# Kernel optimization log

Measured on AMD Instinct MI355X. Metric: run time of the kernel, lower is better.

## Reference

```python
import jax, jax.numpy as jnp
import numpy as np

BN_EPS = 1e-5


def _pool_features(labels, fx, fy, n_labels):
    # Mean-pool per-pixel features (fx, fy, xx, yy coord maps) over superpixel labels.
    B, _, w, h = labels.shape
    xx = (jnp.arange(w, dtype=jnp.float32) / (w - 1)) * 2.0 - 1.0   # varies along dim 2
    yy = (jnp.arange(h, dtype=jnp.float32) / (h - 1)) * 2.0 - 1.0   # varies along dim 3
    xx_map = jnp.broadcast_to(xx[:, None], (w, h))
    yy_map = jnp.broadcast_to(yy[None, :], (w, h))
    P = w * h
    feats = jnp.stack([
        fx[:, 0].reshape(B, P),
        fy[:, 0].reshape(B, P),
        jnp.broadcast_to(xx_map.reshape(1, P), (B, P)),
        jnp.broadcast_to(yy_map.reshape(1, P), (B, P)),
    ], axis=-1).reshape(B * P, 4)                                   # [B*P, 4]
    seg = (labels[:, 0].reshape(B, P)
           + n_labels * jnp.arange(B, dtype=jnp.int32)[:, None]).reshape(-1)
    sums = jax.ops.segment_sum(feats, seg, num_segments=B * n_labels)        # [B*K, 4]
    counts = jax.ops.segment_sum(jnp.ones((B * P,), jnp.float32), seg,
                                 num_segments=B * n_labels)                  # [B*K]
    return sums / jnp.maximum(counts, 1.0)[:, None]


def _bn(x, g, b):
    # BatchNorm1d in training mode: batch statistics over the token dim.
    m = x.mean(axis=0)
    v = x.var(axis=0)
    return (x - m) * jax.lax.rsqrt(v + BN_EPS) * g + b


def reference(labels, fx, fy, frame_idx, n_frames, n_labels,
              conv_w, conv_b, bn1_g, bn1_b, lin_w, lin_b, bn2_g, bn2_b):
    pooled = _pool_features(labels, fx, fy, n_labels)               # [B*K, 4] = (fx, fy, xx, yy)
    t = jnp.repeat(frame_idx.astype(jnp.float32) / (n_frames - 1), n_labels)  # [B*K]
    x = jnp.concatenate([t[:, None], pooled], axis=1)               # [B*K, 5]
    x = x @ conv_w.T + conv_b                                       # Conv1d(5,64,1) == linear
    x = jax.nn.relu(_bn(x, bn1_g, bn1_b))
    x = x @ lin_w.T + lin_b                                         # Linear(64,32)
    x = jax.nn.relu(_bn(x, bn2_g, bn2_b))
    nrm = jnp.linalg.norm(x, axis=1, keepdims=True)
    return x / jnp.maximum(nrm, 1e-8)


def setup_inputs() -> dict:
    key = jax.random.key(0)
    ks = jax.random.split(key, 12)
    B, H, W, K = 16, 512, 512, 1024
    labels = jax.random.randint(ks[0], (B, 1, H, W), 0, K, dtype=jnp.int32)
    fx = jax.random.normal(ks[1], (B, 1, H, W), dtype=jnp.float32)
    fy = jax.random.normal(ks[2], (B, 1, H, W), dtype=jnp.float32)
    frame_idx = jax.random.randint(ks[3], (B,), 0, 100, dtype=jnp.int32)
    conv_w = jax.random.normal(ks[4], (64, 5), dtype=jnp.float32) * 0.3
    conv_b = jax.random.normal(ks[5], (64,), dtype=jnp.float32) * 0.05
    bn1_g = 1.0 + 0.05 * jax.random.normal(ks[6], (64,), dtype=jnp.float32)
    bn1_b = 0.05 * jax.random.normal(ks[7], (64,), dtype=jnp.float32)
    lin_w = jax.random.normal(ks[8], (32, 64), dtype=jnp.float32) * 0.1
    lin_b = jax.random.normal(ks[9], (32,), dtype=jnp.float32) * 0.05
    bn2_g = 1.0 + 0.05 * jax.random.normal(ks[10], (32,), dtype=jnp.float32)
    bn2_b = 0.05 * jax.random.normal(ks[11], (32,), dtype=jnp.float32)
    return {"labels": labels, "fx": fx, "fy": fy, "frame_idx": frame_idx,
            "n_frames": 100, "n_labels": K,
            "conv_w": conv_w, "conv_b": conv_b, "bn1_g": bn1_g, "bn1_b": bn1_b,
            "lin_w": lin_w, "lin_b": lin_b, "bn2_g": bn2_g, "bn2_b": bn2_b}
```

## Files before the change

kernel.cpp:

```cpp
#include <hip/hip_runtime.h>
#include <math.h>

#define TPB 256
#define TPBP 1024
#define FSCALE 16384.0f
#define INV_FSCALE (1.0f / 16384.0f)
#define FBIAS (1 << 17)
#define FCLAMP 7.0f


__global__ __launch_bounds__(TPBP)
void pool_kernel(const int* __restrict__ labels,
                 const float* __restrict__ fx,
                 const float* __restrict__ fy,
                 float* __restrict__ partial,
                 float* __restrict__ ctrl,
                 int K, int H, int W, int wlog, int chunks) {
    extern __shared__ unsigned long long sh[];
    unsigned long long* geo = sh;
    unsigned long long* fxy = sh + K;
    const int tid = threadIdx.x;

    if (blockIdx.x == 0 && tid < 224) ctrl[tid] = 0.f;

    for (int i = tid; i < K; i += TPBP) { geo[i] = 0ull; fxy[i] = 0ull; }
    __syncthreads();

    const int P = H * W;
    const int b = blockIdx.x / chunks;
    const int chunk = blockIdx.x - b * chunks;
    const int chunkP = P / chunks;
    const size_t base = (size_t)b * P + (size_t)chunk * chunkP;
    const int4*   l4p  = (const int4*)(labels + base);
    const float4* fx4p = (const float4*)(fx + base);
    const float4* fy4p = (const float4*)(fy + base);
    const int nvec = chunkP >> 2;

    for (int v = tid; v < nvec; v += TPBP) {
        int4   l4 = l4p[v];
        float4 f4 = fx4p[v];
        float4 g4 = fy4p[v];
        int p0 = chunk * chunkP + (v << 2);
        int   ls[4] = {l4.x, l4.y, l4.z, l4.w};
        float fs[4] = {f4.x, f4.y, f4.z, f4.w};
        float gs[4] = {g4.x, g4.y, g4.z, g4.w};
        #pragma unroll
        for (int s = 0; s < 4; ++s) {
            int p = p0 + s;
            int i, j;
            if (wlog >= 0) { i = p >> wlog; j = p & (W - 1); }
            else           { i = p / W;     j = p - i * W; }
            unsigned long long gadd = ((unsigned long long)i << 40)
                                    | ((unsigned long long)j << 16) | 1ull;
            int qx = __float2int_rn(fminf(fmaxf(fs[s], -FCLAMP), FCLAMP) * FSCALE) + FBIAS;
            int qy = __float2int_rn(fminf(fmaxf(gs[s], -FCLAMP), FCLAMP) * FSCALE) + FBIAS;
            unsigned long long fadd = ((unsigned long long)(unsigned int)qx << 32)
                                    | (unsigned long long)(unsigned int)qy;
            atomicAdd(&geo[ls[s]], gadd);
            atomicAdd(&fxy[ls[s]], fadd);
        }
    }
    __syncthreads();

    const float sx = 2.f / (float)(H - 1);
    const float sy = 2.f / (float)(W - 1);
    float* outp = partial + (size_t)blockIdx.x * K * 5;
    for (int k = tid; k < K; k += TPBP) {
        unsigned long long g = geo[k];
        unsigned long long ff = fxy[k];
        unsigned int ci = (unsigned int)(g & 0xFFFFull);
        float cnt = (float)ci;
        float sj  = (float)(unsigned int)((g >> 16) & 0xFFFFFFull);
        float si  = (float)(unsigned int)(g >> 40);
        long long cbias = (long long)ci << 17;
        float* p = outp + k * 5;
        p[0] = (float)((long long)(ff >> 32) - cbias) * INV_FSCALE;
        p[1] = (float)((long long)(ff & 0xFFFFFFFFull) - cbias) * INV_FSCALE;
        p[2] = sx * si - cnt;
        p[3] = sy * sj - cnt;
        p[4] = cnt;
    }
}

__device__ __forceinline__ void grid_sync(int* cnt, int nblk) {
    __syncthreads();
    if (threadIdx.x == 0) {
        __hip_atomic_fetch_add(cnt, 1, __ATOMIC_RELEASE, __HIP_MEMORY_SCOPE_AGENT);
        while (__hip_atomic_load(cnt, __ATOMIC_RELAXED, __HIP_MEMORY_SCOPE_AGENT) < nblk)
            __builtin_amdgcn_s_sleep(8);
        __hip_atomic_load(cnt, __ATOMIC_ACQUIRE, __HIP_MEMORY_SCOPE_AGENT);
    }
    __syncthreads();
}

__global__ __launch_bounds__(TPB)
void fused234_kernel(const float* __restrict__ partial,
                     const int* __restrict__ frame_idx,
                     const int* __restrict__ n_frames_p,
                     const float* __restrict__ conv_w,
                     const float* __restrict__ conv_b,
                     const float* __restrict__ bn1_g,
                     const float* __restrict__ bn1_b,
                     const float* __restrict__ lin_w,
                     const float* __restrict__ lin_b,
                     const float* __restrict__ bn2_g,
                     const float* __restrict__ bn2_b,
                     float* __restrict__ ctrl,
                     float* __restrict__ statA,
                     float* __restrict__ statB,
                     float* __restrict__ out,
                     int K, int N, int chunks) {
    __shared__ float red[320], feat[320], cw[320], cb[64];
    __shared__ float h1t[64 * 64];
    __shared__ float w2[2048], lb[32];
    __shared__ float sc1[64], sh1[64], sc2[32], sh2[32];
    __shared__ float h2t[32 * 65];
    __shared__ float ssqp[4 * 64], linv[64];

    const int tid = threadIdx.x;
    const int nblk = gridDim.x;
    const int bid = blockIdx.x;
    int* cnt0 = (int*)(ctrl + 192);
    int* cnt1 = (int*)(ctrl + 208);

    for (int i = tid; i < 320; i += TPB) cw[i] = conv_w[i];
    if (tid < 64) cb[tid] = conv_b[tid];
    for (int i = tid; i < 2048; i += TPB) w2[i] = lin_w[i];
    if (tid < 32) lb[tid] = lin_b[tid];

    const int t0 = bid * 64;
    const int b  = t0 / K;
    const int k0 = t0 - b * K;

    float acc0 = 0.f, acc1 = 0.f;
    const float* pb = partial + ((size_t)b * chunks * K + k0) * 5;
    for (int ch = 0; ch < chunks; ++ch) {
        const float* pc = pb + (size_t)ch * K * 5;
        acc0 += pc[tid];
        if (tid < 64) acc1 += pc[256 + tid];
    }
    red[tid] = acc0;
    if (tid < 64) red[256 + tid] = acc1;
    __syncthreads();

    const int g  = tid >> 6;
    const int tt = tid & 63;
    const int t  = t0 + tt;
    const bool valid = t < N;
    if (g == 0) {
        const float* r = red + tt * 5;
        float inv = 1.f / fmaxf(r[4], 1.f);
        float invnf = 1.f / (float)(n_frames_p[0] - 1);
        feat[tt * 5 + 0] = valid ? (float)frame_idx[b] * invnf : 0.f;
        feat[tt * 5 + 1] = r[0] * inv;
        feat[tt * 5 + 2] = r[1] * inv;
        feat[tt * 5 + 3] = r[2] * inv;
        feat[tt * 5 + 4] = r[3] * inv;
    }
    __syncthreads();

    {
        const float x0 = feat[tt * 5 + 0], x1 = feat[tt * 5 + 1],
                    x2 = feat[tt * 5 + 2], x3 = feat[tt * 5 + 3],
                    x4 = feat[tt * 5 + 4];
        float hs[16];
        const int c0 = g * 16;
        #pragma unroll
        for (int j = 0; j < 16; ++j) {
            int c = c0 + j;
            const float* w = cw + c * 5;
            float h = cb[c] + w[0]*x0 + w[1]*x1 + w[2]*x2 + w[3]*x3 + w[4]*x4;
            h1t[c * 64 + tt] = h;
            hs[j] = valid ? h : 0.f;
        }
        float mySum = 0.f, mySq = 0.f;
        #pragma unroll
        for (int j = 0; j < 16; ++j) {
            float s = hs[j];
            float q = hs[j] * hs[j];
            #pragma unroll
            for (int m = 1; m < 64; m <<= 1) {
                s += __shfl_xor(s, m, 64);
                q += __shfl_xor(q, m, 64);
            }
            if (tt == j) { mySum = s; mySq = q; }
        }
        if (tt < 16) {
            statA[(size_t)bid * 128 + c0 + tt] = mySum;
            statA[(size_t)bid * 128 + 64 + c0 + tt] = mySq;
        }
    }

    grid_sync(cnt0, nblk);

    {
        const int col  = tid & 127;
        const int half = tid >> 7;
        float a = 0.f;
        const float* base = statA + (size_t)half * 128 * 128 + col;
        for (int r = 0; r < 128; ++r)
            a += base[(size_t)r * 128];
        red[tid] = a;
    }
    __syncthreads();
    if (tid < 64) {
        float su = red[tid] + red[128 + tid];
        float sq = red[64 + tid] + red[192 + tid];
        float invN = 1.f / (float)N;
        float mean = su * invN;
        float var  = sq * invN - mean * mean;
        float s = bn1_g[tid] * rsqrtf(var + 1e-5f);
        sc1[tid] = s;
        sh1[tid] = bn1_b[tid] - mean * s;
    }
    __syncthreads();

    float y[64];
    #pragma unroll
    for (int c = 0; c < 64; ++c)
        y[c] = fmaxf(h1t[c * 64 + tt] * sc1[c] + sh1[c], 0.f);

    {
        float hs[8];
        const int o0 = g * 8;
        #pragma unroll
        for (int j = 0; j < 8; ++j) {
            int o = o0 + j;
            const float* wo = w2 + o * 64;
            float acc = lb[o];
            #pragma unroll
            for (int c = 0; c < 64; ++c) acc += wo[c] * y[c];
            h2t[o * 65 + tt] = acc;
            hs[j] = valid ? acc : 0.f;
        }
        float mySum = 0.f, mySq = 0.f;
        #pragma unroll
        for (int j = 0; j < 8; ++j) {
            float s = hs[j];
            float q = hs[j] * hs[j];
            #pragma unroll
            for (int m = 1; m < 64; m <<= 1) {
                s += __shfl_xor(s, m, 64);
                q += __shfl_xor(q, m, 64);
            }
            if (tt == j) { mySum = s; mySq = q; }
        }
        if (tt < 8) {
            statB[(size_t)bid * 64 + o0 + tt] = mySum;
            statB[(size_t)bid * 64 + 32 + o0 + tt] = mySq;
        }
    }

    grid_sync(cnt1, nblk);

    {
        const int col = tid & 63;
        const int qr  = tid >> 6;
        float a = 0.f;
        const float* base = statB + (size_t)qr * 64 * 64 + col;
        for (int r = 0; r < 64; ++r)
            a += base[(size_t)r * 64];
        red[tid] = a;
    }
    __syncthreads();
    if (tid < 32) {
        float su = red[tid] + red[64 + tid] + red[128 + tid] + red[192 + tid];
        float sq = red[32 + tid] + red[96 + tid] + red[160 + tid] + red[224 + tid];
        float invN = 1.f / (float)N;
        float mean = su * invN;
        float var  = sq * invN - mean * mean;
        float s = bn2_g[tid] * rsqrtf(var + 1e-5f);
        sc2[tid] = s;
        sh2[tid] = bn2_b[tid] - mean * s;
    }
    __syncthreads();

    {
        const int o0 = g * 8;
        float ss = 0.f;
        #pragma unroll
        for (int j = 0; j < 8; ++j) {
            int o = o0 + j;
            float v = fmaxf(h2t[o * 65 + tt] * sc2[o] + sh2[o], 0.f);
            h2t[o * 65 + tt] = v;
            ss += v * v;
        }
        ssqp[g * 64 + tt] = ss;
    }
    __syncthreads();
    if (g == 0) {
        float tot = ssqp[tt] + ssqp[64 + tt] + ssqp[128 + tt] + ssqp[192 + tt];
        linv[tt] = 1.f / fmaxf(sqrtf(tot), 1e-8f);
    }
    __syncthreads();

    const int nq = min(512, (N - t0) * 8);
    float4* o4 = (float4*)(out + (size_t)t0 * 32);
    for (int q = tid; q < nq; q += TPB) {
        int tk = q >> 3;
        int oo = (q & 7) * 4;
        float iv = linv[tk];
        o4[q] = make_float4(h2t[(oo + 0) * 65 + tk] * iv,
                            h2t[(oo + 1) * 65 + tk] * iv,
                            h2t[(oo + 2) * 65 + tk] * iv,
                            h2t[(oo + 3) * 65 + tk] * iv);
    }
}

extern "C" void kernel_launch(void* const* d_in, const int* in_sizes, int n_in,
                              void* d_out, int out_size, void* d_ws, size_t ws_size,
                              hipStream_t stream) {
    const int*   labels     = (const int*)d_in[0];
    const float* fx         = (const float*)d_in[1];
    const float* fy         = (const float*)d_in[2];
    const int*   frame_idx  = (const int*)d_in[3];
    const int*   n_frames_p = (const int*)d_in[4];
    const float* conv_w = (const float*)d_in[6];
    const float* conv_b = (const float*)d_in[7];
    const float* bn1_g  = (const float*)d_in[8];
    const float* bn1_b  = (const float*)d_in[9];
    const float* lin_w  = (const float*)d_in[10];
    const float* lin_b  = (const float*)d_in[11];
    const float* bn2_g  = (const float*)d_in[12];
    const float* bn2_b  = (const float*)d_in[13];
    float* out = (float*)d_out;

    const int B = in_sizes[3];
    const int P = in_sizes[0] / B;
    const int W = (int)(sqrt((double)P) + 0.5);
    const int H = P / W;
    const int K = out_size / (B * 32);
    const int N = B * K;

    int wlog = -1;
    if ((W & (W - 1)) == 0) { wlog = 0; while ((1 << wlog) < W) ++wlog; }

    const int nblk = (N + 63) / 64;

    float* ctrl    = (float*)d_ws;
    float* statA   = ctrl + 256;
    float* statB   = statA + (size_t)nblk * 128;
    float* partial = statB + (size_t)nblk * 64;

    int chunks = 16;
    while (chunks > 1 && (P % (chunks * 4)) != 0) chunks >>= 1;
    while (P / chunks > 16384) chunks <<= 1;

    pool_kernel<<<B * chunks, TPBP, (size_t)K * 16, stream>>>(
        labels, fx, fy, partial, ctrl, K, H, W, wlog, chunks);
    fused234_kernel<<<nblk, TPB, 0, stream>>>(
        partial, frame_idx, n_frames_p, conv_w, conv_b, bn1_g, bn1_b,
        lin_w, lin_b, bn2_g, bn2_b, ctrl, statA, statB, out, K, N, chunks);
}
```

Before: 152.5 us.

## Replace in-kernel grid barriers with separate kernel launches

Splits the fused MLP/BatchNorm kernel, which used spin-wait grid syncs, into three kernels (layer1, layer2, final). Intermediate activations now go through global memory buffers between launches instead of staying in LDS across the barriers, and the ctrl counter zeroing is dropped. This removes the atomic spin barriers and the co-residency assumption, at the cost of two extra launches and extra global traffic for h1 and h2.

```diff
diff --git a/kernel.cpp b/kernel.cpp
--- a/kernel.cpp
+++ b/kernel.cpp
@@ -14,14 +14,11 @@
                  const float* __restrict__ fx,
                  const float* __restrict__ fy,
                  float* __restrict__ partial,
-                 float* __restrict__ ctrl,
                  int K, int H, int W, int wlog, int chunks) {
     extern __shared__ unsigned long long sh[];
     unsigned long long* geo = sh;
     unsigned long long* fxy = sh + K;
     const int tid = threadIdx.x;
-
-    if (blockIdx.x == 0 && tid < 224) ctrl[tid] = 0.f;
 
     for (int i = tid; i < K; i += TPBP) { geo[i] = 0ull; fxy[i] = 0ull; }
     __syncthreads();
@@ -82,51 +79,22 @@
     }
 }
 
-__device__ __forceinline__ void grid_sync(int* cnt, int nblk) {
-    __syncthreads();
-    if (threadIdx.x == 0) {
-        __hip_atomic_fetch_add(cnt, 1, __ATOMIC_RELEASE, __HIP_MEMORY_SCOPE_AGENT);
-        while (__hip_atomic_load(cnt, __ATOMIC_RELAXED, __HIP_MEMORY_SCOPE_AGENT) < nblk)
-            __builtin_amdgcn_s_sleep(8);
-        __hip_atomic_load(cnt, __ATOMIC_ACQUIRE, __HIP_MEMORY_SCOPE_AGENT);
-    }
-    __syncthreads();
-}
-
 __global__ __launch_bounds__(TPB)
-void fused234_kernel(const float* __restrict__ partial,
-                     const int* __restrict__ frame_idx,
-                     const int* __restrict__ n_frames_p,
-                     const float* __restrict__ conv_w,
-                     const float* __restrict__ conv_b,
-                     const float* __restrict__ bn1_g,
-                     const float* __restrict__ bn1_b,
-                     const float* __restrict__ lin_w,
-                     const float* __restrict__ lin_b,
-                     const float* __restrict__ bn2_g,
-                     const float* __restrict__ bn2_b,
-                     float* __restrict__ ctrl,
-                     float* __restrict__ statA,
-                     float* __restrict__ statB,
-                     float* __restrict__ out,
-                     int K, int N, int chunks) {
+void k_layer1(const float* __restrict__ partial,
+              const int* __restrict__ frame_idx,
+              const int* __restrict__ n_frames_p,
+              const float* __restrict__ conv_w,
+              const float* __restrict__ conv_b,
+              float* __restrict__ statA,
+              float* __restrict__ h1g,
+              int K, int N, int chunks) {
     __shared__ float red[320], feat[320], cw[320], cb[64];
-    __shared__ float h1t[64 * 64];
-    __shared__ float w2[2048], lb[32];
-    __shared__ float sc1[64], sh1[64], sc2[32], sh2[32];
-    __shared__ float h2t[32 * 65];
-    __shared__ float ssqp[4 * 64], linv[64];
 
     const int tid = threadIdx.x;
-    const int nblk = gridDim.x;
     const int bid = blockIdx.x;
-    int* cnt0 = (int*)(ctrl + 192);
-    int* cnt1 = (int*)(ctrl + 208);
 
     for (int i = tid; i < 320; i += TPB) cw[i] = conv_w[i];
     if (tid < 64) cb[tid] = conv_b[tid];
-    for (int i = tid; i < 2048; i += TPB) w2[i] = lin_w[i];
-    if (tid < 32) lb[tid] = lin_b[tid];
 
     const int t0 = bid * 64;
     const int b  = t0 / K;
@@ -159,39 +127,57 @@
     }
     __syncthreads();
 
-    {
-        const float x0 = feat[tt * 5 + 0], x1 = feat[tt * 5 + 1],
-                    x2 = feat[tt * 5 + 2], x3 = feat[tt * 5 + 3],
-                    x4 = feat[tt * 5 + 4];
-        float hs[16];
-        const int c0 = g * 16;
-        #pragma unroll
-        for (int j = 0; j < 16; ++j) {
-            int c = c0 + j;
-            const float* w = cw + c * 5;
-            float h = cb[c] + w[0]*x0 + w[1]*x1 + w[2]*x2 + w[3]*x3 + w[4]*x4;
-            h1t[c * 64 + tt] = h;
-            hs[j] = valid ? h : 0.f;
-        }
-        float mySum = 0.f, mySq = 0.f;
-        #pragma unroll
-        for (int j = 0; j < 16; ++j) {
-            float s = hs[j];
-            float q = hs[j] * hs[j];
-            #pragma unroll
-            for (int m = 1; m < 64; m <<= 1) {
-                s += __shfl_xor(s, m, 64);
-                q += __shfl_xor(q, m, 64);
-            }
-            if (tt == j) { mySum = s; mySq = q; }
-        }
-        if (tt < 16) {
-            statA[(size_t)bid * 128 + c0 + tt] = mySum;
-            statA[(size_t)bid * 128 + 64 + c0 + tt] = mySq;
-        }
-    }
-
-    grid_sync(cnt0, nblk);
+    const float x0 = feat[tt * 5 + 0], x1 = feat[tt * 5 + 1],
+                x2 = feat[tt * 5 + 2], x3 = feat[tt * 5 + 3],
+                x4 = feat[tt * 5 + 4];
+    float hs[16];
+    const int c0 = g * 16;
+    #pragma unroll
+    for (int j = 0; j < 16; ++j) {
+        int c = c0 + j;
+        const float* w = cw + c * 5;
+        float h = cb[c] + w[0]*x0 + w[1]*x1 + w[2]*x2 + w[3]*x3 + w[4]*x4;
+        h1g[(size_t)c * N + t] = h;
+        hs[j] = valid ? h : 0.f;
+    }
+    float mySum = 0.f, mySq = 0.f;
+    #pragma unroll
+    for (int j = 0; j < 16; ++j) {
+        float s = hs[j];
+        float q = hs[j] * hs[j];
+        #pragma unroll
+        for (int m = 1; m < 64; m <<= 1) {
+            s += __shfl_xor(s, m, 64);
+            q += __shfl_xor(q, m, 64);
+        }
+        if (tt == j) { mySum = s; mySq = q; }
+    }
+    if (tt < 16) {
+        statA[(size_t)bid * 128 + c0 + tt] = mySum;
+        statA[(size_t)bid * 128 + 64 + c0 + tt] = mySq;
+    }
+}
+
+__global__ __launch_bounds__(TPB)
+void k_layer2(const float* __restrict__ statA,
+              const float* __restrict__ bn1_g,
+              const float* __restrict__ bn1_b,
+              const float* __restrict__ lin_w,
+              const float* __restrict__ lin_b,
+              const float* __restrict__ h1g,
+              float* __restrict__ statB,
+              float* __restrict__ h2g,
+              int N) {
+    __shared__ float red[320], w2[2048], lb[32];
+    __shared__ float sc1[64], sh1[64];
+    __shared__ float h1t[64 * 64];
+
+    const int tid = threadIdx.x;
+    const int bid = blockIdx.x;
+    const int t0 = bid * 64;
+
+    for (int i = tid; i < 2048; i += TPB) w2[i] = lin_w[i];
+    if (tid < 32) lb[tid] = lin_b[tid];
 
     {
         const int col  = tid & 127;
@@ -202,7 +188,18 @@
             a += base[(size_t)r * 128];
         red[tid] = a;
     }
-    __syncthreads();
+
+    {
+        #pragma unroll
+        for (int pass = 0; pass < 4; ++pass) {
+            int idx = pass * TPB + tid;
+            int c = idx >> 4, q = idx & 15;
+            float4 v = *(const float4*)(h1g + (size_t)c * N + t0 + q * 4);
+            *(float4*)(&h1t[c * 64 + q * 4]) = v;
+        }
+    }
+    __syncthreads();
+
     if (tid < 64) {
         float su = red[tid] + red[128 + tid];
         float sq = red[64 + tid] + red[192 + tid];
@@ -215,43 +212,61 @@
     }
     __syncthreads();
 
+    const int g  = tid >> 6;
+    const int tt = tid & 63;
+    const int t  = t0 + tt;
+    const bool valid = t < N;
+
     float y[64];
     #pragma unroll
     for (int c = 0; c < 64; ++c)
         y[c] = fmaxf(h1t[c * 64 + tt] * sc1[c] + sh1[c], 0.f);
 
-    {
-        float hs[8];
-        const int o0 = g * 8;
-        #pragma unroll
-        for (int j = 0; j < 8; ++j) {
-            int o = o0 + j;
-            const float* wo = w2 + o * 64;
-            float acc = lb[o];
-            #pragma unroll
-            for (int c = 0; c < 64; ++c) acc += wo[c] * y[c];
-            h2t[o * 65 + tt] = acc;
-            hs[j] = valid ? acc : 0.f;
-        }
-        float mySum = 0.f, mySq = 0.f;
-        #pragma unroll
-        for (int j = 0; j < 8; ++j) {
-            float s = hs[j];
-            float q = hs[j] * hs[j];
-            #pragma unroll
-            for (int m = 1; m < 64; m <<= 1) {
-                s += __shfl_xor(s, m, 64);
-                q += __shfl_xor(q, m, 64);
-            }
-            if (tt == j) { mySum = s; mySq = q; }
-        }
-        if (tt < 8) {
-            statB[(size_t)bid * 64 + o0 + tt] = mySum;
-            statB[(size_t)bid * 64 + 32 + o0 + tt] = mySq;
-        }
-    }
-
-    grid_sync(cnt1, nblk);
+    float hs[8];
+    const int o0 = g * 8;
+    #pragma unroll
+    for (int j = 0; j < 8; ++j) {
+        int o = o0 + j;
+        const float* wo = w2 + o * 64;
+        float acc = lb[o];
+        #pragma unroll
+        for (int c = 0; c < 64; ++c) acc += wo[c] * y[c];
+        h2g[(size_t)o * N + t] = acc;
+        hs[j] = valid ? acc : 0.f;
+    }
+    float mySum = 0.f, mySq = 0.f;
+    #pragma unroll
+    for (int j = 0; j < 8; ++j) {
+        float s = hs[j];
+        float q = hs[j] * hs[j];
+        #pragma unroll
+        for (int m = 1; m < 64; m <<= 1) {
+            s += __shfl_xor(s, m, 64);
+            q += __shfl_xor(q, m, 64);
+        }
+        if (tt == j) { mySum = s; mySq = q; }
+    }
+    if (tt < 8) {
+        statB[(size_t)bid * 64 + o0 + tt] = mySum;
+        statB[(size_t)bid * 64 + 32 + o0 + tt] = mySq;
+    }
+}
+
+__global__ __launch_bounds__(TPB)
+void k_final(const float* __restrict__ statB,
+             const float* __restrict__ bn2_g,
+             const float* __restrict__ bn2_b,
+             const float* __restrict__ h2g,
+             float* __restrict__ out,
+             int N) {
+    __shared__ float red[256];
+    __shared__ float sc2[32], sh2[32];
+    __shared__ float h2t[32 * 68];
+    __shared__ float ssqp[4 * 64], linv[64];
+
+    const int tid = threadIdx.x;
+    const int bid = blockIdx.x;
+    const int t0 = bid * 64;
 
     {
         const int col = tid & 63;
@@ -262,7 +277,18 @@
             a += base[(size_t)r * 64];
         red[tid] = a;
     }
-    __syncthreads();
+
+    {
+        #pragma unroll
+        for (int pass = 0; pass < 2; ++pass) {
+            int idx = pass * TPB + tid;
+            int o = idx >> 4, q = idx & 15;
+            float4 v = *(const float4*)(h2g + (size_t)o * N + t0 + q * 4);
+            *(float4*)(&h2t[o * 68 + q * 4]) = v;
+        }
+    }
+    __syncthreads();
+
     if (tid < 32) {
         float su = red[tid] + red[64 + tid] + red[128 + tid] + red[192 + tid];
         float sq = red[32 + tid] + red[96 + tid] + red[160 + tid] + red[224 + tid];
@@ -275,14 +301,16 @@
     }
     __syncthreads();
 
+    const int g  = tid >> 6;
+    const int tt = tid & 63;
     {
         const int o0 = g * 8;
         float ss = 0.f;
         #pragma unroll
         for (int j = 0; j < 8; ++j) {
             int o = o0 + j;
-            float v = fmaxf(h2t[o * 65 + tt] * sc2[o] + sh2[o], 0.f);
-            h2t[o * 65 + tt] = v;
+            float v = fmaxf(h2t[o * 68 + tt] * sc2[o] + sh2[o], 0.f);
+            h2t[o * 68 + tt] = v;
             ss += v * v;
         }
         ssqp[g * 64 + tt] = ss;
@@ -300,10 +328,10 @@
         int tk = q >> 3;
         int oo = (q & 7) * 4;
         float iv = linv[tk];
-        o4[q] = make_float4(h2t[(oo + 0) * 65 + tk] * iv,
-                            h2t[(oo + 1) * 65 + tk] * iv,
-                            h2t[(oo + 2) * 65 + tk] * iv,
-                            h2t[(oo + 3) * 65 + tk] * iv);
+        o4[q] = make_float4(h2t[(oo + 0) * 68 + tk] * iv,
+                            h2t[(oo + 1) * 68 + tk] * iv,
+                            h2t[(oo + 2) * 68 + tk] * iv,
+                            h2t[(oo + 3) * 68 + tk] * iv);
     }
 }
 
@@ -337,18 +365,22 @@
 
     const int nblk = (N + 63) / 64;
 
-    float* ctrl    = (float*)d_ws;
-    float* statA   = ctrl + 256;
-    float* statB   = statA + (size_t)nblk * 128;
-    float* partial = statB + (size_t)nblk * 64;
-
     int chunks = 16;
     while (chunks > 1 && (P % (chunks * 4)) != 0) chunks >>= 1;
     while (P / chunks > 16384) chunks <<= 1;
 
+    float* statA   = (float*)d_ws;
+    float* statB   = statA + (size_t)nblk * 128;
+    float* partial = statB + (size_t)nblk * 64;
+    float* h1g     = partial + (size_t)B * chunks * K * 5;
+    float* h2g     = h1g + (size_t)64 * N;
+
     pool_kernel<<<B * chunks, TPBP, (size_t)K * 16, stream>>>(
-        labels, fx, fy, partial, ctrl, K, H, W, wlog, chunks);
-    fused234_kernel<<<nblk, TPB, 0, stream>>>(
-        partial, frame_idx, n_frames_p, conv_w, conv_b, bn1_g, bn1_b,
-        lin_w, lin_b, bn2_g, bn2_b, ctrl, statA, statB, out, K, N, chunks);
-}
+        labels, fx, fy, partial, K, H, W, wlog, chunks);
+    k_layer1<<<nblk, TPB, 0, stream>>>(
+        partial, frame_idx, n_frames_p, conv_w, conv_b, statA, h1g, K, N, chunks);
+    k_layer2<<<nblk, TPB, 0, stream>>>(
+        statA, bn1_g, bn1_b, lin_w, lin_b, h1g, statB, h2g, N);
+    k_final<<<nblk, TPB, 0, stream>>>(
+        statB, bn2_g, bn2_b, h2g, out, N);
+}
```

After: 133.1 us. 1.15x faster.
